# Kernel optimization log

Measured on AMD Instinct MI355X. Metric: run time of the kernel, lower is better.

Reference implementation:

```python
import jax, jax.numpy as jnp
import numpy as np

EPS = 1e-7  # keras.backend.epsilon()


def setup_inputs() -> dict:
    key = jax.random.key(0)
    k1, k2 = jax.random.split(key)
    B, S, D = 8, 1024, 768
    # scale down: module exponentiates raw dot products with no max-subtraction
    input_a = jax.random.normal(k1, (B, S, D), dtype=jnp.float32) * 0.05
    input_mask = jax.random.randint(k2, (B, S), 0, 2, dtype=jnp.int32)
    return {"input_a": input_a, "input_mask": input_mask}


def reference(input_a, input_mask):
    # e = exp(Q K^T) with Q = K = input_a, attend_type='dot' (no scaling)
    e = jnp.exp(jnp.einsum('bsd,btd->bst', input_a, input_a))  # [B,S,S]
    m = input_mask.astype(input_a.dtype)
    e = e * m[:, :, None] * m[:, None, :]  # mask rows and cols
    e = e / (jnp.sum(e, axis=-1, keepdims=True) + EPS)  # renormalize
    attend = jnp.einsum('bst,btd->bsd', e, input_a)  # V = input_a
    return attend
```

## Files before the change

kernel.cpp:

```cpp
#include <hip/hip_runtime.h>
#include <cstdint>
#include <cstddef>

#define BATCH 8
#define SEQ 1024
#define DIM 768
#define EPS_K 1e-7f

typedef __bf16 bf16x8 __attribute__((ext_vector_type(8)));
typedef float f32x4 __attribute__((ext_vector_type(4)));

__device__ __forceinline__ uint16_t f2bf(float f) {
  union { float f; uint32_t u; } v; v.f = f;
  uint32_t u = v.u;
  u += 0x7FFFu + ((u >> 16) & 1u);
  return (uint16_t)(u >> 16);
}

__device__ __forceinline__ void gload16(const void* g, void* l) {
  __builtin_amdgcn_global_load_lds(
      (const __attribute__((address_space(1))) uint32_t*)g,
      (__attribute__((address_space(3))) uint32_t*)l, 16, 0, 0);
}

__global__ __launch_bounds__(256) void convert_kernel(const float* __restrict__ A,
                                                      uint16_t* __restrict__ ab,
                                                      uint16_t* __restrict__ at) {
  const int b  = blockIdx.z;
  const int s0 = blockIdx.y * 64;
  const int d0 = blockIdx.x * 64;
  __shared__ uint16_t tl[64][66];
  const int c  = threadIdx.x & 63;
  const int r0 = threadIdx.x >> 6;
  const float* Ab = A + (size_t)b * SEQ * DIM;
  uint16_t* abb = ab + (size_t)b * SEQ * DIM;
#pragma unroll
  for (int i = 0; i < 16; ++i) {
    int r = r0 + i * 4;
    uint16_t h = f2bf(Ab[(size_t)(s0 + r) * DIM + d0 + c]);
    abb[(size_t)(s0 + r) * DIM + d0 + c] = h;
    tl[r][c] = h;
  }
  __syncthreads();
  uint16_t* atb = at + (size_t)b * DIM * SEQ;
#pragma unroll
  for (int i = 0; i < 16; ++i) {
    int r = r0 + i * 4;
    atb[(size_t)(d0 + r) * SEQ + s0 + c] = tl[c][r];
  }
}

__global__ __launch_bounds__(256) void scores_kernel(const uint16_t* __restrict__ ab,
                                                     const int* __restrict__ mask,
                                                     uint16_t* __restrict__ P,
                                                     float* __restrict__ den) {
  const int b   = blockIdx.z;
  const int s0  = blockIdx.y * 128;
  const int t0  = blockIdx.x * 128;
  const int tid = threadIdx.x;
  const int lane = tid & 63;
  const int wid  = tid >> 6;
  const int wr   = wid >> 1;
  const int wc   = wid & 1;

  __shared__ uint16_t ldsQ[128 * 32];
  __shared__ uint16_t ldsK[128 * 32];
  __shared__ float mrow[128];
  __shared__ float mcol[128];

  if (tid < 128)        mrow[tid]       = (float)mask[b * SEQ + s0 + tid];
  else                  mcol[tid - 128] = (float)mask[b * SEQ + t0 + (tid - 128)];

  const uint16_t* aQ = ab + (size_t)b * SEQ * DIM + (size_t)s0 * DIM;
  const uint16_t* aK = ab + (size_t)b * SEQ * DIM + (size_t)t0 * DIM;

  f32x4 acc[4][4];
#pragma unroll
  for (int m = 0; m < 4; ++m)
#pragma unroll
    for (int n = 0; n < 4; ++n) acc[m][n] = f32x4{0.f, 0.f, 0.f, 0.f};

  for (int k0 = 0; k0 < DIM; k0 += 32) {
    __syncthreads();
#pragma unroll
    for (int i = 0; i < 2; ++i) {
      int idx = (i * 256 + tid) * 8;
      int r = idx >> 5, c = idx & 31;
      gload16(aQ + (size_t)r * DIM + k0 + c, &ldsQ[idx]);
      gload16(aK + (size_t)r * DIM + k0 + c, &ldsK[idx]);
    }
    __syncthreads();

    bf16x8 qf[4], kf[4];
    const int rowQ = wr * 64 + (lane & 15);
    const int rowK = wc * 64 + (lane & 15);
    const int kch  = (lane >> 4) * 8;
#pragma unroll
    for (int m = 0; m < 4; ++m) qf[m] = *(const bf16x8*)&ldsQ[(rowQ + m * 16) * 32 + kch];
#pragma unroll
    for (int n = 0; n < 4; ++n) kf[n] = *(const bf16x8*)&ldsK[(rowK + n * 16) * 32 + kch];
#pragma unroll
    for (int m = 0; m < 4; ++m)
#pragma unroll
      for (int n = 0; n < 4; ++n)
        acc[m][n] = __builtin_amdgcn_mfma_f32_16x16x32_bf16(qf[m], kf[n], acc[m][n], 0, 0, 0);
  }

  uint16_t* Pb = P + (size_t)b * SEQ * SEQ;
#pragma unroll
  for (int m = 0; m < 4; ++m) {
#pragma unroll
    for (int j = 0; j < 4; ++j) {
      const int ql = wr * 64 + m * 16 + (lane >> 4) * 4 + j;
      const int q  = s0 + ql;
      const float mr = mrow[ql];
      float rs = 0.f;
#pragma unroll
      for (int n = 0; n < 4; ++n) {
        const int tl = wc * 64 + n * 16 + (lane & 15);
        float e = __expf(acc[m][n][j]) * mr * mcol[tl];
        rs += e;
        Pb[(size_t)q * SEQ + t0 + tl] = f2bf(e);
      }
      rs += __shfl_xor(rs, 1);
      rs += __shfl_xor(rs, 2);
      rs += __shfl_xor(rs, 4);
      rs += __shfl_xor(rs, 8);
      if ((lane & 15) == 0) atomicAdd(&den[b * SEQ + q], rs);
    }
  }
}

__global__ __launch_bounds__(256) void out_kernel(const uint16_t* __restrict__ P,
                                                  const uint16_t* __restrict__ at,
                                                  const float* __restrict__ den,
                                                  float* __restrict__ out) {
  const int b   = blockIdx.z;
  const int q0  = blockIdx.y * 128;
  const int d0  = blockIdx.x * 128;
  const int tid = threadIdx.x;
  const int lane = tid & 63;
  const int wid  = tid >> 6;
  const int wr   = wid >> 1;
  const int wc   = wid & 1;

  __shared__ uint16_t ldsP[128 * 32];
  __shared__ uint16_t ldsA[128 * 32];
  __shared__ float rden[128];

  if (tid < 128) rden[tid] = 1.0f / (den[b * SEQ + q0 + tid] + EPS_K);

  const uint16_t* Pb = P  + (size_t)b * SEQ * SEQ + (size_t)q0 * SEQ;
  const uint16_t* Ab = at + (size_t)b * DIM * SEQ + (size_t)d0 * SEQ;

  f32x4 acc[4][4];
#pragma unroll
  for (int m = 0; m < 4; ++m)
#pragma unroll
    for (int n = 0; n < 4; ++n) acc[m][n] = f32x4{0.f, 0.f, 0.f, 0.f};

  for (int k0 = 0; k0 < SEQ; k0 += 32) {
    __syncthreads();
#pragma unroll
    for (int i = 0; i < 2; ++i) {
      int idx = (i * 256 + tid) * 8;
      int r = idx >> 5, c = idx & 31;
      gload16(Pb + (size_t)r * SEQ + k0 + c, &ldsP[idx]);
      gload16(Ab + (size_t)r * SEQ + k0 + c, &ldsA[idx]);
    }
    __syncthreads();

    bf16x8 pf[4], af[4];
    const int rowP = wr * 64 + (lane & 15);
    const int rowA = wc * 64 + (lane & 15);
    const int kch  = (lane >> 4) * 8;
#pragma unroll
    for (int m = 0; m < 4; ++m) pf[m] = *(const bf16x8*)&ldsP[(rowP + m * 16) * 32 + kch];
#pragma unroll
    for (int n = 0; n < 4; ++n) af[n] = *(const bf16x8*)&ldsA[(rowA + n * 16) * 32 + kch];
#pragma unroll
    for (int m = 0; m < 4; ++m)
#pragma unroll
      for (int n = 0; n < 4; ++n)
        acc[m][n] = __builtin_amdgcn_mfma_f32_16x16x32_bf16(pf[m], af[n], acc[m][n], 0, 0, 0);
  }

  float* ob = out + (size_t)b * SEQ * DIM;
#pragma unroll
  for (int m = 0; m < 4; ++m) {
#pragma unroll
    for (int j = 0; j < 4; ++j) {
      const int ql = wr * 64 + m * 16 + (lane >> 4) * 4 + j;
      const float sc = rden[ql];
#pragma unroll
      for (int n = 0; n < 4; ++n) {
        const int dl = d0 + wc * 64 + n * 16 + (lane & 15);
        ob[(size_t)(q0 + ql) * DIM + dl] = acc[m][n][j] * sc;
      }
    }
  }
}

extern "C" void kernel_launch(void* const* d_in, const int* in_sizes, int n_in,
                              void* d_out, int out_size, void* d_ws, size_t ws_size,
                              hipStream_t stream) {
  (void)in_sizes; (void)n_in; (void)out_size; (void)ws_size;
  const float* A    = (const float*)d_in[0];
  const int*   mask = (const int*)d_in[1];
  float*       out  = (float*)d_out;

  char* ws = (char*)d_ws;
  const size_t NB_AB = (size_t)BATCH * SEQ * DIM * 2;
  const size_t NB_AT = NB_AB;
  const size_t NB_P  = (size_t)BATCH * SEQ * SEQ * 2;
  uint16_t* ab  = (uint16_t*)(ws);
  uint16_t* at  = (uint16_t*)(ws + NB_AB);
  uint16_t* P   = (uint16_t*)(ws + NB_AB + NB_AT);
  float*    den = (float*)   (ws + NB_AB + NB_AT + NB_P);

  dim3 blk(256);
  convert_kernel<<<dim3(DIM / 64, SEQ / 64, BATCH), blk, 0, stream>>>(A, ab, at);
  hipMemsetAsync(den, 0, (size_t)BATCH * SEQ * sizeof(float), stream);
  scores_kernel<<<dim3(SEQ / 128, SEQ / 128, BATCH), blk, 0, stream>>>(ab, mask, P, den);
  out_kernel<<<dim3(DIM / 128, SEQ / 128, BATCH), blk, 0, stream>>>(P, at, den, out);
}
```

Baseline: 132.9 us.

## Exploit symmetry of A·Aᵀ to compute only upper-triangle score tiles

Because Q and K are the same matrix, the score matrix is symmetric, so the scores kernel now launches only the 36 upper-triangle 128x128 tiles per batch and writes each off-diagonal tile's transpose as well. Column sums are accumulated and atomically added to the denominators for the mirrored rows. The denominator zeroing is folded into the convert kernel, removing the separate memset. This roughly halves the QKᵀ matmul and exp work, at the cost of strided transposed stores and more atomics.

```diff
diff --git a/kernel.cpp b/kernel.cpp
--- a/kernel.cpp
+++ b/kernel.cpp
@@ -9,6 +9,7 @@
 
 typedef __bf16 bf16x8 __attribute__((ext_vector_type(8)));
 typedef float f32x4 __attribute__((ext_vector_type(4)));
+typedef uint16_t u16x4 __attribute__((ext_vector_type(4)));
 
 __device__ __forceinline__ uint16_t f2bf(float f) {
   union { float f; uint32_t u; } v; v.f = f;
@@ -25,13 +26,15 @@
 
 __global__ __launch_bounds__(256) void convert_kernel(const float* __restrict__ A,
                                                       uint16_t* __restrict__ ab,
-                                                      uint16_t* __restrict__ at) {
+                                                      uint16_t* __restrict__ at,
+                                                      float* __restrict__ den) {
   const int b  = blockIdx.z;
   const int s0 = blockIdx.y * 64;
   const int d0 = blockIdx.x * 64;
   __shared__ uint16_t tl[64][66];
   const int c  = threadIdx.x & 63;
   const int r0 = threadIdx.x >> 6;
+  if (blockIdx.x == 0 && threadIdx.x < 64) den[b * SEQ + s0 + threadIdx.x] = 0.f;
   const float* Ab = A + (size_t)b * SEQ * DIM;
   uint16_t* abb = ab + (size_t)b * SEQ * DIM;
 #pragma unroll
@@ -54,10 +57,16 @@
                                                      const int* __restrict__ mask,
                                                      uint16_t* __restrict__ P,
                                                      float* __restrict__ den) {
-  const int b   = blockIdx.z;
-  const int s0  = blockIdx.y * 128;
-  const int t0  = blockIdx.x * 128;
-  const int tid = threadIdx.x;
+  const int b = blockIdx.z;
+  int rem = blockIdx.x, ti = 0;
+#pragma unroll
+  for (int it = 0; it < 8; ++it) { if (rem >= 8 - ti) { rem -= 8 - ti; ++ti; } }
+  const int tj   = ti + rem;
+  const int s0   = ti * 128;
+  const int t0   = tj * 128;
+  const bool diag = (ti == tj);
+
+  const int tid  = threadIdx.x;
   const int lane = tid & 63;
   const int wid  = tid >> 6;
   const int wr   = wid >> 1;
@@ -107,26 +116,46 @@
   }
 
   uint16_t* Pb = P + (size_t)b * SEQ * SEQ;
+  float colAcc[4] = {0.f, 0.f, 0.f, 0.f};
 #pragma unroll
   for (int m = 0; m < 4; ++m) {
+    float rsj[4] = {0.f, 0.f, 0.f, 0.f};
+    const int qb = wr * 64 + m * 16 + (lane >> 4) * 4;
+#pragma unroll
+    for (int n = 0; n < 4; ++n) {
+      const int tloc = wc * 64 + n * 16 + (lane & 15);
+      const float mc = mcol[tloc];
+      u16x4 tr;
+#pragma unroll
+      for (int j = 0; j < 4; ++j) {
+        float e = __expf(acc[m][n][j]) * mrow[qb + j] * mc;
+        rsj[j]    += e;
+        colAcc[n] += e;
+        uint16_t h = f2bf(e);
+        tr[j] = h;
+        Pb[(size_t)(s0 + qb + j) * SEQ + t0 + tloc] = h;
+      }
+      if (!diag) {
+        *(u16x4*)&Pb[(size_t)(t0 + tloc) * SEQ + s0 + qb] = tr;
+      }
+    }
 #pragma unroll
     for (int j = 0; j < 4; ++j) {
-      const int ql = wr * 64 + m * 16 + (lane >> 4) * 4 + j;
-      const int q  = s0 + ql;
-      const float mr = mrow[ql];
-      float rs = 0.f;
-#pragma unroll
-      for (int n = 0; n < 4; ++n) {
-        const int tl = wc * 64 + n * 16 + (lane & 15);
-        float e = __expf(acc[m][n][j]) * mr * mcol[tl];
-        rs += e;
-        Pb[(size_t)q * SEQ + t0 + tl] = f2bf(e);
-      }
+      float rs = rsj[j];
       rs += __shfl_xor(rs, 1);
       rs += __shfl_xor(rs, 2);
       rs += __shfl_xor(rs, 4);
       rs += __shfl_xor(rs, 8);
-      if ((lane & 15) == 0) atomicAdd(&den[b * SEQ + q], rs);
+      if ((lane & 15) == 0) atomicAdd(&den[b * SEQ + s0 + qb + j], rs);
+    }
+  }
+  if (!diag) {
+#pragma unroll
+    for (int n = 0; n < 4; ++n) {
+      float cs = colAcc[n];
+      cs += __shfl_xor(cs, 16);
+      cs += __shfl_xor(cs, 32);
+      if (lane < 16) atomicAdd(&den[b * SEQ + t0 + wc * 64 + n * 16 + lane], cs);
     }
   }
 }
@@ -219,8 +248,7 @@
   float*    den = (float*)   (ws + NB_AB + NB_AT + NB_P);
 
   dim3 blk(256);
-  convert_kernel<<<dim3(DIM / 64, SEQ / 64, BATCH), blk, 0, stream>>>(A, ab, at);
-  hipMemsetAsync(den, 0, (size_t)BATCH * SEQ * sizeof(float), stream);
-  scores_kernel<<<dim3(SEQ / 128, SEQ / 128, BATCH), blk, 0, stream>>>(ab, mask, P, den);
+  convert_kernel<<<dim3(DIM / 64, SEQ / 64, BATCH), blk, 0, stream>>>(A, ab, at, den);
+  scores_kernel<<<dim3(36, 1, BATCH), blk, 0, stream>>>(ab, mask, P, den);
   out_kernel<<<dim3(DIM / 128, SEQ / 128, BATCH), blk, 0, stream>>>(P, at, den, out);
 }
```

Result: no change. 134.7 us (+1.4%).

## Double-buffer LDS staging and compute row sums via MFMA with ones vector

Applied to the files above, without the earlier changes.

Both GEMM kernels now double-buffer their LDS tiles, prefetching the next K-slice while the current one feeds MFMA, which halves the barriers per iteration. The row-sum denominator is no longer built with shuffles and atomics in the scores kernel. Instead the output kernel gets it with an extra MFMA of P against a ones vector, which removes the memset, the atomics and the den buffer. The grids are flattened with batch as the fastest index so concurrent blocks spread across batches. The costs are doubled LDS use, about 25% more MFMA work in the output kernel, and a denominator summed from bf16-rounded P values.

```diff
diff --git a/kernel.cpp b/kernel.cpp
--- a/kernel.cpp
+++ b/kernel.cpp
@@ -52,19 +52,20 @@
 
 __global__ __launch_bounds__(256) void scores_kernel(const uint16_t* __restrict__ ab,
                                                      const int* __restrict__ mask,
-                                                     uint16_t* __restrict__ P,
-                                                     float* __restrict__ den) {
-  const int b   = blockIdx.z;
-  const int s0  = blockIdx.y * 128;
-  const int t0  = blockIdx.x * 128;
-  const int tid = threadIdx.x;
+                                                     uint16_t* __restrict__ P) {
+  const int b    = blockIdx.x & 7;
+  const int tile = blockIdx.x >> 3;
+  const int s0   = (tile >> 3) * 128;
+  const int t0   = (tile & 7) * 128;
+
+  const int tid  = threadIdx.x;
   const int lane = tid & 63;
   const int wid  = tid >> 6;
   const int wr   = wid >> 1;
   const int wc   = wid & 1;
 
-  __shared__ uint16_t ldsQ[128 * 32];
-  __shared__ uint16_t ldsK[128 * 32];
+  __shared__ uint16_t ldsQ[2][128 * 32];
+  __shared__ uint16_t ldsK[2][128 * 32];
   __shared__ float mrow[128];
   __shared__ float mcol[128];
 
@@ -74,116 +75,139 @@
   const uint16_t* aQ = ab + (size_t)b * SEQ * DIM + (size_t)s0 * DIM;
   const uint16_t* aK = ab + (size_t)b * SEQ * DIM + (size_t)t0 * DIM;
 
+  const int sr = (tid * 8) >> 5;
+  const int sc = (tid * 8) & 31;
+#define STAGE(buf, k0)                                                         \
+  do {                                                                         \
+    int _i0 = tid * 8, _i1 = (256 + tid) * 8;                                  \
+    gload16(aQ + (size_t)sr * DIM + (k0) + sc,        &ldsQ[buf][_i0]);        \
+    gload16(aQ + (size_t)(sr + 64) * DIM + (k0) + sc, &ldsQ[buf][_i1]);        \
+    gload16(aK + (size_t)sr * DIM + (k0) + sc,        &ldsK[buf][_i0]);        \
+    gload16(aK + (size_t)(sr + 64) * DIM + (k0) + sc, &ldsK[buf][_i1]);        \
+  } while (0)
+
   f32x4 acc[4][4];
 #pragma unroll
   for (int m = 0; m < 4; ++m)
 #pragma unroll
     for (int n = 0; n < 4; ++n) acc[m][n] = f32x4{0.f, 0.f, 0.f, 0.f};
 
+  STAGE(0, 0);
+  __syncthreads();
+
+  const int rowQ = wr * 64 + (lane & 15);
+  const int rowK = wc * 64 + (lane & 15);
+  const int kch  = (lane >> 4) * 8;
+
+  int cur = 0;
   for (int k0 = 0; k0 < DIM; k0 += 32) {
-    __syncthreads();
-#pragma unroll
-    for (int i = 0; i < 2; ++i) {
-      int idx = (i * 256 + tid) * 8;
-      int r = idx >> 5, c = idx & 31;
-      gload16(aQ + (size_t)r * DIM + k0 + c, &ldsQ[idx]);
-      gload16(aK + (size_t)r * DIM + k0 + c, &ldsK[idx]);
-    }
-    __syncthreads();
+    if (k0 + 32 < DIM) STAGE(cur ^ 1, k0 + 32);
 
     bf16x8 qf[4], kf[4];
-    const int rowQ = wr * 64 + (lane & 15);
-    const int rowK = wc * 64 + (lane & 15);
-    const int kch  = (lane >> 4) * 8;
-#pragma unroll
-    for (int m = 0; m < 4; ++m) qf[m] = *(const bf16x8*)&ldsQ[(rowQ + m * 16) * 32 + kch];
-#pragma unroll
-    for (int n = 0; n < 4; ++n) kf[n] = *(const bf16x8*)&ldsK[(rowK + n * 16) * 32 + kch];
+#pragma unroll
+    for (int m = 0; m < 4; ++m) qf[m] = *(const bf16x8*)&ldsQ[cur][(rowQ + m * 16) * 32 + kch];
+#pragma unroll
+    for (int n = 0; n < 4; ++n) kf[n] = *(const bf16x8*)&ldsK[cur][(rowK + n * 16) * 32 + kch];
 #pragma unroll
     for (int m = 0; m < 4; ++m)
 #pragma unroll
       for (int n = 0; n < 4; ++n)
         acc[m][n] = __builtin_amdgcn_mfma_f32_16x16x32_bf16(qf[m], kf[n], acc[m][n], 0, 0, 0);
-  }
+
+    __syncthreads();
+    cur ^= 1;
+  }
+#undef STAGE
 
   uint16_t* Pb = P + (size_t)b * SEQ * SEQ;
 #pragma unroll
   for (int m = 0; m < 4; ++m) {
-#pragma unroll
-    for (int j = 0; j < 4; ++j) {
-      const int ql = wr * 64 + m * 16 + (lane >> 4) * 4 + j;
-      const int q  = s0 + ql;
-      const float mr = mrow[ql];
-      float rs = 0.f;
-#pragma unroll
-      for (int n = 0; n < 4; ++n) {
-        const int tl = wc * 64 + n * 16 + (lane & 15);
-        float e = __expf(acc[m][n][j]) * mr * mcol[tl];
-        rs += e;
-        Pb[(size_t)q * SEQ + t0 + tl] = f2bf(e);
+    const int qb = wr * 64 + m * 16 + (lane >> 4) * 4;
+#pragma unroll
+    for (int n = 0; n < 4; ++n) {
+      const int tloc = wc * 64 + n * 16 + (lane & 15);
+      const float mc = mcol[tloc];
+#pragma unroll
+      for (int j = 0; j < 4; ++j) {
+        float e = __expf(acc[m][n][j]) * mrow[qb + j] * mc;
+        Pb[(size_t)(s0 + qb + j) * SEQ + t0 + tloc] = f2bf(e);
       }
-      rs += __shfl_xor(rs, 1);
-      rs += __shfl_xor(rs, 2);
-      rs += __shfl_xor(rs, 4);
-      rs += __shfl_xor(rs, 8);
-      if ((lane & 15) == 0) atomicAdd(&den[b * SEQ + q], rs);
     }
   }
 }
 
 __global__ __launch_bounds__(256) void out_kernel(const uint16_t* __restrict__ P,
                                                   const uint16_t* __restrict__ at,
-                                                  const float* __restrict__ den,
                                                   float* __restrict__ out) {
-  const int b   = blockIdx.z;
-  const int q0  = blockIdx.y * 128;
-  const int d0  = blockIdx.x * 128;
-  const int tid = threadIdx.x;
+  const int b    = blockIdx.x & 7;
+  const int tile = blockIdx.x >> 3;
+  const int q0   = (tile / 6) * 128;
+  const int d0   = (tile % 6) * 128;
+
+  const int tid  = threadIdx.x;
   const int lane = tid & 63;
   const int wid  = tid >> 6;
   const int wr   = wid >> 1;
   const int wc   = wid & 1;
 
-  __shared__ uint16_t ldsP[128 * 32];
-  __shared__ uint16_t ldsA[128 * 32];
-  __shared__ float rden[128];
-
-  if (tid < 128) rden[tid] = 1.0f / (den[b * SEQ + q0 + tid] + EPS_K);
+  __shared__ uint16_t ldsP[2][128 * 32];
+  __shared__ uint16_t ldsA[2][128 * 32];
 
   const uint16_t* Pb = P  + (size_t)b * SEQ * SEQ + (size_t)q0 * SEQ;
   const uint16_t* Ab = at + (size_t)b * DIM * SEQ + (size_t)d0 * SEQ;
 
+  const int sr = (tid * 8) >> 5;
+  const int sc = (tid * 8) & 31;
+#define STAGE(buf, k0)                                                         \
+  do {                                                                         \
+    int _i0 = tid * 8, _i1 = (256 + tid) * 8;                                  \
+    gload16(Pb + (size_t)sr * SEQ + (k0) + sc,        &ldsP[buf][_i0]);        \
+    gload16(Pb + (size_t)(sr + 64) * SEQ + (k0) + sc, &ldsP[buf][_i1]);        \
+    gload16(Ab + (size_t)sr * SEQ + (k0) + sc,        &ldsA[buf][_i0]);        \
+    gload16(Ab + (size_t)(sr + 64) * SEQ + (k0) + sc, &ldsA[buf][_i1]);        \
+  } while (0)
+
   f32x4 acc[4][4];
-#pragma unroll
-  for (int m = 0; m < 4; ++m)
+  f32x4 accd[4];
+#pragma unroll
+  for (int m = 0; m < 4; ++m) {
+    accd[m] = f32x4{0.f, 0.f, 0.f, 0.f};
 #pragma unroll
     for (int n = 0; n < 4; ++n) acc[m][n] = f32x4{0.f, 0.f, 0.f, 0.f};
-
+  }
+
+  bf16x8 onesf;
+#pragma unroll
+  for (int i = 0; i < 8; ++i) onesf[i] = (__bf16)1.0f;
+
+  STAGE(0, 0);
+  __syncthreads();
+
+  const int rowP = wr * 64 + (lane & 15);
+  const int rowA = wc * 64 + (lane & 15);
+  const int kch  = (lane >> 4) * 8;
+
+  int cur = 0;
   for (int k0 = 0; k0 < SEQ; k0 += 32) {
-    __syncthreads();
-#pragma unroll
-    for (int i = 0; i < 2; ++i) {
-      int idx = (i * 256 + tid) * 8;
-      int r = idx >> 5, c = idx & 31;
-      gload16(Pb + (size_t)r * SEQ + k0 + c, &ldsP[idx]);
-      gload16(Ab + (size_t)r * SEQ + k0 + c, &ldsA[idx]);
-    }
-    __syncthreads();
+    if (k0 + 32 < SEQ) STAGE(cur ^ 1, k0 + 32);
 
     bf16x8 pf[4], af[4];
-    const int rowP = wr * 64 + (lane & 15);
-    const int rowA = wc * 64 + (lane & 15);
-    const int kch  = (lane >> 4) * 8;
-#pragma unroll
-    for (int m = 0; m < 4; ++m) pf[m] = *(const bf16x8*)&ldsP[(rowP + m * 16) * 32 + kch];
-#pragma unroll
-    for (int n = 0; n < 4; ++n) af[n] = *(const bf16x8*)&ldsA[(rowA + n * 16) * 32 + kch];
-#pragma unroll
-    for (int m = 0; m < 4; ++m)
+#pragma unroll
+    for (int m = 0; m < 4; ++m) pf[m] = *(const bf16x8*)&ldsP[cur][(rowP + m * 16) * 32 + kch];
+#pragma unroll
+    for (int n = 0; n < 4; ++n) af[n] = *(const bf16x8*)&ldsA[cur][(rowA + n * 16) * 32 + kch];
+#pragma unroll
+    for (int m = 0; m < 4; ++m) {
 #pragma unroll
       for (int n = 0; n < 4; ++n)
         acc[m][n] = __builtin_amdgcn_mfma_f32_16x16x32_bf16(pf[m], af[n], acc[m][n], 0, 0, 0);
-  }
+      accd[m] = __builtin_amdgcn_mfma_f32_16x16x32_bf16(pf[m], onesf, accd[m], 0, 0, 0);
+    }
+
+    __syncthreads();
+    cur ^= 1;
+  }
+#undef STAGE
 
   float* ob = out + (size_t)b * SEQ * DIM;
 #pragma unroll
@@ -191,11 +215,11 @@
 #pragma unroll
     for (int j = 0; j < 4; ++j) {
       const int ql = wr * 64 + m * 16 + (lane >> 4) * 4 + j;
-      const float sc = rden[ql];
+      const float sc2 = 1.0f / (accd[m][j] + EPS_K);
 #pragma unroll
       for (int n = 0; n < 4; ++n) {
         const int dl = d0 + wc * 64 + n * 16 + (lane & 15);
-        ob[(size_t)(q0 + ql) * DIM + dl] = acc[m][n][j] * sc;
+        ob[(size_t)(q0 + ql) * DIM + dl] = acc[m][n][j] * sc2;
       }
     }
   }
@@ -212,15 +236,12 @@
   char* ws = (char*)d_ws;
   const size_t NB_AB = (size_t)BATCH * SEQ * DIM * 2;
   const size_t NB_AT = NB_AB;
-  const size_t NB_P  = (size_t)BATCH * SEQ * SEQ * 2;
-  uint16_t* ab  = (uint16_t*)(ws);
-  uint16_t* at  = (uint16_t*)(ws + NB_AB);
-  uint16_t* P   = (uint16_t*)(ws + NB_AB + NB_AT);
-  float*    den = (float*)   (ws + NB_AB + NB_AT + NB_P);
+  uint16_t* ab = (uint16_t*)(ws);
+  uint16_t* at = (uint16_t*)(ws + NB_AB);
+  uint16_t* P  = (uint16_t*)(ws + NB_AB + NB_AT);
 
   dim3 blk(256);
   convert_kernel<<<dim3(DIM / 64, SEQ / 64, BATCH), blk, 0, stream>>>(A, ab, at);
-  hipMemsetAsync(den, 0, (size_t)BATCH * SEQ * sizeof(float), stream);
-  scores_kernel<<<dim3(SEQ / 128, SEQ / 128, BATCH), blk, 0, stream>>>(ab, mask, P, den);
-  out_kernel<<<dim3(DIM / 128, SEQ / 128, BATCH), blk, 0, stream>>>(P, at, den, out);
-}
+  scores_kernel<<<dim3(64 * BATCH), blk, 0, stream>>>(ab, mask, P);
+  out_kernel<<<dim3(48 * BATCH), blk, 0, stream>>>(P, at, out);
+}
```

After: 118.6 us. 1.12x faster.
